# Performance work log

Measured on AMD Instinct MI355X. Metric: run time of the kernel, lower is better.

The kernel has to match this reference:

```python
import jax, jax.numpy as jnp
import numpy as np

HEAD, DIM, R = 8, 256, 3
RA = (2 * R + 1) ** 2  # 49


def conv2d(x, w, b=None, pad=0, groups=1):
    y = jax.lax.conv_general_dilated(x, w, (1, 1), [(pad, pad), (pad, pad)],
                                     dimension_numbers=('NCHW', 'OIHW', 'NCHW'),
                                     feature_group_count=groups)
    return y if b is None else y + b[None, :, None, None]


def grid_sample(img, grid, mode, padding='zeros'):
    # img [B,C,H,W]; grid [B,Hg,Wg,2] with (x,y) in [-1,1]; align_corners=False.
    B, C, H, W = img.shape
    Hg, Wg = grid.shape[1], grid.shape[2]
    gx = ((grid[..., 0] + 1.0) * W - 1.0) / 2.0
    gy = ((grid[..., 1] + 1.0) * H - 1.0) / 2.0
    if padding == 'border':
        gx = jnp.clip(gx, 0.0, W - 1.0)
        gy = jnp.clip(gy, 0.0, H - 1.0)
    gx = gx.reshape(B, -1)
    gy = gy.reshape(B, -1)

    def gather(iy, ix):
        iyc = jnp.clip(iy, 0, H - 1)
        ixc = jnp.clip(ix, 0, W - 1)
        return jax.vmap(lambda im, a, b: im[:, a, b])(img, iyc, ixc)  # [B,C,N]

    def mask(iy, ix):
        if padding == 'border':
            return jnp.ones(iy.shape, img.dtype)
        return ((ix >= 0) & (ix < W) & (iy >= 0) & (iy < H)).astype(img.dtype)

    if mode == 'nearest':
        ix = jnp.round(gx).astype(jnp.int32)
        iy = jnp.round(gy).astype(jnp.int32)
        out = gather(iy, ix) * mask(iy, ix)[:, None, :]
    else:  # bilinear
        x0f = jnp.floor(gx); y0f = jnp.floor(gy)
        wx = gx - x0f; wy = gy - y0f
        x0 = x0f.astype(jnp.int32); y0 = y0f.astype(jnp.int32)
        out = jnp.zeros((B, C, gx.shape[1]), img.dtype)
        for dx, dy, w in ((0, 0, (1 - wx) * (1 - wy)), (1, 0, wx * (1 - wy)),
                          (0, 1, (1 - wx) * wy), (1, 1, wx * wy)):
            ix = x0 + dx; iy = y0 + dy
            out = out + gather(iy, ix) * (w * mask(iy, ix))[:, None, :]
    return out.reshape(B, C, Hg, Wg)


def mlp2(x, W1, b1, W2, b2):
    return jax.nn.relu(x @ W1.T + b1) @ W2.T + b2


def setup_inputs() -> dict:
    key = jax.random.key(0)
    ks = jax.random.split(key, 32)
    B, H, W, Q = 1, 64, 64, 4096
    f32 = jnp.float32
    rn = lambda k, shp, s=0.02: jax.random.normal(k, shp, f32) * s
    return {
        'inp': jax.random.normal(ks[0], (B, 3, H, W), f32),
        'coord': jax.random.uniform(ks[1], (B, Q, 2), f32, -1.0, 1.0),
        'cell': jnp.full((B, Q, 2), 2.0 / (2 * H), f32),
        'W_enc': rn(ks[2], (64, 3, 3, 3)), 'b_enc': jnp.zeros((64,), f32),
        'W_ch': rn(ks[3], (256, 64, 3, 3)), 'b_ch': jnp.zeros((256,), f32),
        'W_q': rn(ks[4], (256, 256, 3, 3)), 'b_q': jnp.zeros((256,), f32),
        'W_k': rn(ks[5], (256, 256, 3, 3)), 'b_k': jnp.zeros((256,), f32),
        'W_v': rn(ks[6], (256, 256, 3, 3)), 'b_v': jnp.zeros((256,), f32),
        'W_off1': rn(ks[7], (256, 32, 5, 5)), 'b_off1': jnp.zeros((256,), f32),
        'ln_g': jnp.ones((256,), f32), 'ln_b': jnp.zeros((256,), f32),
        'W_off2': rn(ks[8], (98, 256, 1, 1)),
        'Wc1': rn(ks[9], (256, 98)), 'bc1': jnp.zeros((256,), f32),
        'Wc2': rn(ks[10], (49, 256)), 'bc2': jnp.zeros((49,), f32),
        'Wi1': rn(ks[11], (256, 12546)), 'bi1': jnp.zeros((256,), f32),
        'Wi2': rn(ks[12], (3, 256)), 'bi2': jnp.zeros((3,), f32),
        'scale': 2,
    }


def reference(inp, coord, cell, W_enc, b_enc, W_ch, b_ch, W_q, b_q, W_k, b_k,
              W_v, b_v, W_off1, b_off1, ln_g, ln_b, W_off2, Wc1, bc1, Wc2, bc2,
              Wi1, bi1, Wi2, bi2, scale):
    B, _, H, W = inp.shape
    Q = coord.shape[1]
    # gen_feat: encoder stub (conv+relu) -> conv_ch -> q/k/v convs
    feat = conv2d(jax.nn.relu(conv2d(inp, W_enc, b_enc, pad=1)), W_ch, b_ch, pad=1)
    fq = conv2d(feat, W_q, b_q, pad=1)
    fk = conv2d(feat, W_k, b_k, pad=1)
    fv = conv2d(feat, W_v, b_v, pad=1)
    # offset branch: grouped 5x5 conv -> channelwise LN -> GELU -> 1x1 conv (no bias)
    o = conv2d(feat, W_off1, b_off1, pad=2, groups=8)
    oc = o.transpose(0, 2, 3, 1)
    mu = oc.mean(-1, keepdims=True)
    var = ((oc - mu) ** 2).mean(-1, keepdims=True)
    oc = (oc - mu) / jnp.sqrt(var + 1e-5) * ln_g + ln_b
    offsets = conv2d(jax.nn.gelu(oc.transpose(0, 3, 1, 2), approximate=False), W_off2, None, pad=0)  # [B,98,H,W]
    # LR coordinate grid (y,x) at pixel centers in [-1,1]
    ys = -1.0 + 1.0 / H + (2.0 / H) * jnp.arange(H, dtype=inp.dtype)
    xs = -1.0 + 1.0 / W + (2.0 / W) * jnp.arange(W, dtype=inp.dtype)
    coord_lr = jnp.broadcast_to(jnp.stack(jnp.meshgrid(ys, xs, indexing='ij'), 0)[None], (B, 2, H, W))
    sc = coord[:, :, None, :]          # [B,Q,1,2] (y,x)
    g = sc[..., ::-1]                  # (x,y) for grid_sample
    sck = grid_sample(coord_lr, g, 'nearest').transpose(0, 2, 3, 1)  # [B,Q,1,2]
    off = grid_sample(offsets, g, 'nearest').transpose(0, 2, 3, 1).reshape(B, Q, RA, 2)
    off = jnp.tanh(off) * jnp.array([1.0 / (H - 1.0), 1.0 / (W - 1.0)], inp.dtype) * 2.0
    d = jnp.linspace(-R, R, 2 * R + 1).astype(inp.dtype)
    delta = jnp.stack(jnp.meshgrid(d * (2.0 / H), d * (2.0 / W), indexing='ij'), -1).reshape(1, 1, RA, 2)
    sck = sck + delta + off            # [B,Q,49,2] sampling locs (y,x)
    q = grid_sample(fq, g, 'bilinear').transpose(0, 2, 3, 1).reshape(B, Q, HEAD, DIM // HEAD)
    k = grid_sample(fk, sck[..., ::-1], 'nearest').transpose(0, 2, 3, 1).reshape(B, Q, RA, HEAD, DIM // HEAD)
    v = grid_sample(fv, sck[..., ::-1], 'nearest').transpose(0, 2, 3, 1).reshape(B, Q, RA, HEAD, DIM // HEAD)
    attn_val = jnp.einsum('bqhd,bqkhd->bqkh', q, k) / np.sqrt(DIM // HEAD)  # [B,Q,49,8]
    rel = (sc - sck) * jnp.array([H, W], inp.dtype)  # [B,Q,49,2]
    wcoord = mlp2(rel.reshape(B * Q, RA * 2), Wc1, bc1, Wc2, bc2).reshape(B, Q, RA, 1)
    attn = jax.nn.softmax(wcoord + attn_val, axis=2)  # softmax over 49 samples
    feat_in = (v * attn[..., None]).reshape(B, Q, RA * DIM)
    rel_cell = cell * jnp.array([H, W], inp.dtype)
    feat_in = jnp.concatenate([feat_in, rel_cell], -1)  # [B,Q,12546]
    pred = mlp2(feat_in.reshape(B * Q, -1), Wi1, bi1, Wi2, bi2).reshape(B, Q, 3)
    skip = grid_sample(inp, g, 'bilinear', 'border')[:, :, :, 0].transpose(0, 2, 1)
    return pred + skip
```

## Files before the change

kernel.cpp:

```cpp
#include <hip/hip_runtime.h>
#include <hip/hip_bf16.h>


typedef unsigned short u16;
typedef unsigned int u32;
using frag_ab = __attribute__((ext_vector_type(8))) short;
using frag_cd = __attribute__((ext_vector_type(4))) float;

#define HW 4096
#define NQ 4096
#define KBIG 12576
#define SPLITK 16
#define KCHUNK 800
#define JMAX 5
#define KQ 2304
#define QSPLIT 3
#define QCHUNK 768
#define NBLK_QKV (64 * 6 * QSPLIT)
#define NBLK_OFF1 (64 * 8)

static __device__ __forceinline__ u16 f2b(float f) {
  union { __hip_bfloat16 h; u16 u; } c; c.h = __float2bfloat16(f); return c.u;
}
static __device__ __forceinline__ float b2f(u16 v) {
  return __uint_as_float((u32)v << 16);
}
static __device__ __forceinline__ u32 pk2(float a, float b) {
  union { __hip_bfloat162 h; u32 u; } c;
  c.h = __float22bfloat162_rn(float2{a, b});
  return c.u;
}
static __device__ __forceinline__ void glds16(const u16* g, u16* l) {
  __builtin_amdgcn_global_load_lds(
      (const __attribute__((address_space(1))) u32*)(g),
      (__attribute__((address_space(3))) u32*)(l), 16, 0, 0);
}

#define BM 64
#define BN 64
#define BK 32
#define LDSS 40

__global__ __launch_bounds__(256)
void gemm_feat(const u16* __restrict__ feat, const u16* __restrict__ Btqkv,
               u16* __restrict__ Pq, const u16* __restrict__ Btoff1,
               float* __restrict__ obuf, const float* __restrict__ b_off1)
{
  __shared__ u16 smem[6656];
  const int bid = blockIdx.x;
  const int tid = threadIdx.x;
  const int wave = tid >> 6, lane = tid & 63;
  const int lr = lane & 15, lk = lane >> 4;

  if (bid < NBLK_QKV) {
    u16* As = smem;
    u16* Bs = smem + 64 * 40;
    const int mz  = bid & 63;
    const int rest = bid >> 6;
    const int ny  = rest % 6;
    const int z   = rest / 6;
    const int m0  = mz * 64;
    const int n0  = ny * 128;
    const int kbeg = z * QCHUNK;
    const int kend = kbeg + QCHUNK;
    const int nw = wave * 32;
    const int arow = tid >> 2, acol = (tid & 3) * 8;
    const int p = m0 + arow, y = p >> 6, x = p & 63;

    frag_cd acc[4][2] = {};
    const u16* bbase = Btqkv + (size_t)(n0 + (tid >> 2)) * KQ + (tid & 3) * 8 + kbeg;
    u16* bdst = &Bs[(size_t)tid * 8];

    auto stageA = [&](int k0) -> uint4 {
      int k = k0 + acol;
      int s = k >> 8, c = k & 255;
      int dy = s / 3, dx = s - dy * 3;
      int yy = y + dy - 1, xx = x + dx - 1;
      if (((unsigned)yy < 64u) && ((unsigned)xx < 64u))
        return *(const uint4*)&feat[(size_t)(yy * 64 + xx) * 256 + c];
      return uint4{0u, 0u, 0u, 0u};
    };

    uint4 av = stageA(kbeg);

    for (int k0 = kbeg; k0 < kend; k0 += BK) {
      glds16(bbase + (k0 - kbeg), bdst);
      glds16(bbase + (k0 - kbeg) + (size_t)64 * KQ, bdst + 2048);
      *(uint4*)&As[arow * LDSS + acol] = av;
      __syncthreads();
      if (k0 + BK < kend) av = stageA(k0 + BK);
      frag_ab af[4];
      #pragma unroll
      for (int i = 0; i < 4; i++)
        af[i] = *(const frag_ab*)&As[(i * 16 + lr) * LDSS + lk * 8];
      #pragma unroll
      for (int j = 0; j < 2; j++) {
        frag_ab bf = *(const frag_ab*)&Bs[(nw + j * 16 + lr) * 32 + lk * 8];
        #pragma unroll
        for (int i = 0; i < 4; i++)
          acc[i][j] = __builtin_amdgcn_mfma_f32_16x16x32_bf16(af[i], bf, acc[i][j], 0, 0, 0);
      }
      __syncthreads();
    }

    #pragma unroll
    for (int i = 0; i < 4; i++)
      #pragma unroll
      for (int j = 0; j < 2; j++) {
        int col = n0 + nw + j * 16 + lr;
        #pragma unroll
        for (int r = 0; r < 4; r++) {
          int row = m0 + i * 16 + lk * 4 + r;
          Pq[(size_t)z * (NQ * 768) + (size_t)row * 768 + col] = f2b(acc[i][j][r]);
        }
      }
  } else {
    u16* As = smem;
    u16* Bs = smem + 64 * 40;
    const int t  = bid - NBLK_QKV;
    const int m0 = (t & 63) * 64;
    const int g  = t >> 6;
    const int cb = g * 32;
    const u16* Bt = Btoff1 + (size_t)g * 32 * 800;
    const float* bz = b_off1 + g * 32;
    const int mw = (wave & 1) * 32, nw = (wave >> 1) * 32;
    const int srow = tid >> 2, scol = (tid & 3) * 8;
    const int p = m0 + srow, y = p >> 6, x = p & 63;

    frag_cd acc[2][2] = {};
    const bool bok  = srow < 32;
    const u16* bptr = Bt + (size_t)srow * 800 + scol;

    auto stageA = [&](int k0) -> uint4 {
      int k = k0 + scol;
      int s = k >> 5;
      int c = k & 31;
      int dy = s / 5, dx = s - dy * 5;
      int yy = y + dy - 2, xx = x + dx - 2;
      if (((unsigned)yy < 64u) && ((unsigned)xx < 64u))
        return *(const uint4*)&feat[(size_t)(yy * 64 + xx) * 256 + cb + c];
      return uint4{0u, 0u, 0u, 0u};
    };

    uint4 av = stageA(0);
    uint4 bv = bok ? *(const uint4*)(bptr) : uint4{0u, 0u, 0u, 0u};

    for (int k0 = 0; k0 < 800; k0 += BK) {
      *(uint4*)&As[srow * LDSS + scol] = av;
      *(uint4*)&Bs[srow * LDSS + scol] = bv;
      __syncthreads();
      if (k0 + BK < 800) {
        av = stageA(k0 + BK);
        bv = bok ? *(const uint4*)(bptr + k0 + BK) : uint4{0u, 0u, 0u, 0u};
      }
      frag_ab af0 = *(const frag_ab*)&As[(mw      + lr) * LDSS + lk * 8];
      frag_ab af1 = *(const frag_ab*)&As[(mw + 16 + lr) * LDSS + lk * 8];
      frag_ab bf0 = *(const frag_ab*)&Bs[(nw      + lr) * LDSS + lk * 8];
      frag_ab bf1 = *(const frag_ab*)&Bs[(nw + 16 + lr) * LDSS + lk * 8];
      acc[0][0] = __builtin_amdgcn_mfma_f32_16x16x32_bf16(af0, bf0, acc[0][0], 0, 0, 0);
      acc[0][1] = __builtin_amdgcn_mfma_f32_16x16x32_bf16(af0, bf1, acc[0][1], 0, 0, 0);
      acc[1][0] = __builtin_amdgcn_mfma_f32_16x16x32_bf16(af1, bf0, acc[1][0], 0, 0, 0);
      acc[1][1] = __builtin_amdgcn_mfma_f32_16x16x32_bf16(af1, bf1, acc[1][1], 0, 0, 0);
      __syncthreads();
    }

    #pragma unroll
    for (int i = 0; i < 2; i++)
      #pragma unroll
      for (int j = 0; j < 2; j++) {
        int col = nw + j * 16 + lr;
        if (col >= 32) continue;
        float badd = bz[col];
        #pragma unroll
        for (int r = 0; r < 4; r++) {
          int row = m0 + mw + i * 16 + lk * 4 + r;
          obuf[(size_t)row * 256 + g * 32 + col] = acc[i][j][r] + badd;
        }
      }
  }
}

#define RQ_BLKS 1536
#define LNO_BLKS 256
__global__ __launch_bounds__(256)
void post_feat(const u16* __restrict__ P, const float* __restrict__ bias,
               u16* __restrict__ outQ, u16* __restrict__ outK,
               u16* __restrict__ outV,
               const float* __restrict__ x, const float* __restrict__ g,
               const float* __restrict__ b, const u16* __restrict__ Btoff2,
               float* __restrict__ offsb)
{
  __shared__ u16 s_oc[16 * 264];
  const int bid = blockIdx.x;
  const int tid = threadIdx.x;
  if (bid < RQ_BLKS) {
    int i8 = bid * 256 + tid;
    size_t i = (size_t)i8 * 8;
    int row = (int)(i / 768);
    int c = (int)(i % 768);
    float v[8];
    #pragma unroll
    for (int t = 0; t < 8; t++) v[t] = bias[c + t];
    for (int z = 0; z < QSPLIT; z++) {
      uint4 a = *(const uint4*)&P[(size_t)z * (NQ * 768) + i];
      u32 aw[4] = {a.x, a.y, a.z, a.w};
      #pragma unroll
      for (int t = 0; t < 4; t++) {
        v[2 * t]     += __uint_as_float(aw[t] << 16);
        v[2 * t + 1] += __uint_as_float(aw[t] & 0xffff0000u);
      }
    }
    uint4 ob = {pk2(v[0], v[1]), pk2(v[2], v[3]), pk2(v[4], v[5]), pk2(v[6], v[7])};
    if (c < 256) {
      *(uint4*)&outQ[(size_t)row * 256 + c] = ob;
    } else if (c < 512) {
      *(uint4*)&outK[(size_t)row * 256 + (c - 256)] = ob;
    } else {
      *(uint4*)&outV[(size_t)row * 256 + (c - 512)] = ob;
    }
  } else {
    const int p0 = (bid - RQ_BLKS) * 16;
    const int p = tid >> 4, gl = tid & 15;
    float v[16];
    {
      const float* src = x + (size_t)(p0 + p) * 256 + gl * 16;
      #pragma unroll
      for (int t = 0; t < 4; t++) {
        float4 f = *(const float4*)(src + t * 4);
        v[4 * t] = f.x; v[4 * t + 1] = f.y; v[4 * t + 2] = f.z; v[4 * t + 3] = f.w;
      }
    }
    float s1 = 0.f, s2 = 0.f;
    #pragma unroll
    for (int t = 0; t < 16; t++) { s1 += v[t]; s2 += v[t] * v[t]; }
    #pragma unroll
    for (int off = 8; off; off >>= 1) {
      s1 += __shfl_xor(s1, off, 16);
      s2 += __shfl_xor(s2, off, 16);
    }
    float mu   = s1 * (1.f / 256.f);
    float var  = s2 * (1.f / 256.f) - mu * mu;
    float rstd = rsqrtf(var + 1e-5f);
    #pragma unroll
    for (int t = 0; t < 16; t++) {
      int c = gl * 16 + t;
      float xn = (v[t] - mu) * rstd * g[c] + b[c];
      float ge = 0.5f * xn * (1.f + erff(xn * 0.70710678118654752f));
      s_oc[p * 264 + c] = f2b(ge);
    }
    __syncthreads();
    const int wave = tid >> 6, lane = tid & 63;
    const int lr = lane & 15, lk = lane >> 4;
    frag_cd a0 = {}, a1 = {};
    #pragma unroll
    for (int k0 = 0; k0 < 256; k0 += 32) {
      frag_ab af = *(const frag_ab*)&s_oc[lr * 264 + k0 + lk * 8];
      frag_ab bf0 = *(const frag_ab*)&Btoff2[(size_t)(wave * 16 + lr) * 256 + k0 + lk * 8];
      a0 = __builtin_amdgcn_mfma_f32_16x16x32_bf16(af, bf0, a0, 0, 0, 0);
      if (wave < 3) {
        frag_ab bf1 = *(const frag_ab*)&Btoff2[(size_t)((wave + 4) * 16 + lr) * 256 + k0 + lk * 8];
        a1 = __builtin_amdgcn_mfma_f32_16x16x32_bf16(af, bf1, a1, 0, 0, 0);
      }
    }
    {
      const int col0 = wave * 16 + lr;
      const int col1 = (wave + 4) * 16 + lr;
      #pragma unroll
      for (int r = 0; r < 4; r++) {
        int row = lk * 4 + r;
        offsb[(size_t)(p0 + row) * 98 + col0] = a0[r];
        if (wave < 3 && col1 < 98)
          offsb[(size_t)(p0 + row) * 98 + col1] = a1[r];
      }
    }
  }
}

__global__ __launch_bounds__(512, 4)
void gemm_big(const u16* __restrict__ Bt, const u16* __restrict__ fqkvV,
              const float* __restrict__ attnval, const int* __restrict__ vidx,
              const float* __restrict__ cell, u16* __restrict__ P)
{
  __shared__ u16 As[128 * LDSS];
  __shared__ u16 Bs[2 * 256 * 32];
  __shared__ short s_vidx[JMAX * 128];
  __shared__ float s_attn[JMAX * 128 * 8];
  const int tid  = threadIdx.x;
  const int m0   = blockIdx.x * 128;
  const int z    = blockIdx.y;
  const int kbeg = z * KCHUNK;
  const int kend = min(KBIG, kbeg + KCHUNK);
  const int jbeg = kbeg >> 8;
  const int jcnt = ((kend - 1) >> 8) - jbeg + 1;
  const int wave = tid >> 6, lane = tid & 63;
  const int mw = (wave & 1) * 64, nwv = (wave >> 1) * 64;
  const int lr = lane & 15, lk = lane >> 4;
  const int arow = tid >> 2, acol = (tid & 3) * 8;
  const int q = m0 + arow;

  for (int t = tid; t < 128 * jcnt; t += 512) {
    int r = t & 127, jj = t >> 7;
    int j = jbeg + jj;
    s_vidx[t] = (short)((j < 49) ? vidx[(m0 + r) * 49 + j] : -1);
  }
  for (int t = tid; t < 128 * 8 * jcnt; t += 512) {
    int h = t & 7, rr = (t >> 3) & 127, jj = t >> 10;
    int j = jbeg + jj;
    s_attn[t] = (j < 49) ? attnval[((size_t)((m0 + rr) * 49 + j)) * 8 + h] : 0.f;
  }
  __syncthreads();

  auto loadA = [&](int k0, uint4& kv, float& w) {
    const int k = k0 + acol;
    const int j = k >> 8, c = k & 255;
    kv = uint4{0u, 0u, 0u, 0u};
    w = 0.f;
    if (j < 49) {
      const int jj = j - jbeg;
      int id = s_vidx[jj * 128 + arow];
      if (id >= 0) {
        w = s_attn[(jj * 128 + arow) * 8 + (c >> 5)];
        kv = *(const uint4*)(fqkvV + (size_t)id * 256 + c);
      }
    } else if (c == 0) {
      kv.x = pk2(cell[q * 2], cell[q * 2 + 1]);
      w = 64.f;
    }
  };

  frag_cd acc[4][4] = {};
  uint4 kvc; float wc_;
  const u16* bbase = Bt + (size_t)(tid >> 2) * KBIG + (tid & 3) * 8 + kbeg;

  glds16(bbase, &Bs[(size_t)tid * 8]);
  glds16(bbase + (size_t)128 * KBIG, &Bs[(size_t)tid * 8 + 4096]);
  loadA(kbeg, kvc, wc_);

  int par = 0;
  for (int k0 = kbeg; k0 < kend; k0 += BK, par ^= 1) {
    {
      u32 aw[4] = {kvc.x, kvc.y, kvc.z, kvc.w};
      uint4 av;
      u32 avw[4];
      #pragma unroll
      for (int t = 0; t < 4; t++) {
        float lo = __uint_as_float(aw[t] << 16) * wc_;
        float hi = __uint_as_float(aw[t] & 0xffff0000u) * wc_;
        avw[t] = pk2(lo, hi);
      }
      av.x = avw[0]; av.y = avw[1]; av.z = avw[2]; av.w = avw[3];
      *(uint4*)&As[arow * LDSS + acol] = av;
    }
    if (k0 + BK < kend) {
      u16* bd = &Bs[(size_t)(par ^ 1) * 8192 + (size_t)tid * 8];
      glds16(bbase + (k0 + BK - kbeg), bd);
      glds16(bbase + (k0 + BK - kbeg) + (size_t)128 * KBIG, bd + 4096);
      asm volatile("s_waitcnt vmcnt(2) lgkmcnt(0)" ::: "memory");
    } else {
      asm volatile("s_waitcnt vmcnt(0) lgkmcnt(0)" ::: "memory");
    }
    __builtin_amdgcn_s_barrier();
    if (k0 + BK < kend) loadA(k0 + BK, kvc, wc_);
    const u16* bsrc = &Bs[(size_t)par * 8192];
    frag_ab af[4];
    #pragma unroll
    for (int i = 0; i < 4; i++)
      af[i] = *(const frag_ab*)&As[(mw + i * 16 + lr) * LDSS + lk * 8];
    #pragma unroll
    for (int j = 0; j < 4; j++) {
      frag_ab bf = *(const frag_ab*)&bsrc[(nwv + j * 16 + lr) * 32 + lk * 8];
      #pragma unroll
      for (int i = 0; i < 4; i++)
        acc[i][j] = __builtin_amdgcn_mfma_f32_16x16x32_bf16(af[i], bf, acc[i][j], 0, 0, 0);
    }
    asm volatile("s_waitcnt lgkmcnt(0)" ::: "memory");
    __builtin_amdgcn_s_barrier();
  }

  #pragma unroll
  for (int i = 0; i < 4; i++)
    #pragma unroll
    for (int j = 0; j < 4; j++) {
      int col = nwv + j * 16 + lr;
      #pragma unroll
      for (int r = 0; r < 4; r++) {
        int row = m0 + mw + i * 16 + lk * 4 + r;
        P[(size_t)z * (NQ * 256) + (size_t)row * 256 + col] = f2b(acc[i][j][r]);
      }
    }
}

__global__ __launch_bounds__(256)
void reduce_final(const u16* __restrict__ Pb, const float* __restrict__ bi1,
                  const float* __restrict__ Wi2, const float* __restrict__ bi2,
                  const float* __restrict__ skipb, float* __restrict__ out)
{
  const int q = blockIdx.x, c = threadIdx.x;
  float s = 0.f;
  #pragma unroll
  for (int z = 0; z < SPLITK; z++)
    s += b2f(Pb[(size_t)z * (NQ * 256) + (size_t)q * 256 + c]);
  s += bi1[c];
  s = fmaxf(s, 0.f);

  __shared__ float part[3][4];
  float p0 = s * Wi2[c], p1 = s * Wi2[256 + c], p2 = s * Wi2[512 + c];
  #pragma unroll
  for (int off = 32; off; off >>= 1) {
    p0 += __shfl_xor(p0, off);
    p1 += __shfl_xor(p1, off);
    p2 += __shfl_xor(p2, off);
  }
  if ((c & 63) == 0) {
    int w = c >> 6;
    part[0][w] = p0; part[1][w] = p1; part[2][w] = p2;
  }
  __syncthreads();
  if (c < 3)
    out[q * 3 + c] = bi2[c] + skipb[q * 3 + c]
                   + part[c][0] + part[c][1] + part[c][2] + part[c][3];
}

__global__ __launch_bounds__(256)
void attn_wc(const u16* __restrict__ relbuf, const u16* __restrict__ Btc1,
             const float* __restrict__ bc1, const u16* __restrict__ Btc2,
             const float* __restrict__ bc2, float* __restrict__ attnval)
{
  __shared__ u16 s_rel[16 * 136];
  __shared__ u16 s_hid[16 * 264];
  __shared__ float s_wc[16 * 52];
  const int tid = threadIdx.x;
  const int m0 = blockIdx.x * 16;
  const int wave = tid >> 6, lane = tid & 63;
  const int lr = lane & 15, lk = lane >> 4;

  {
    int r = tid >> 4, kc = (tid & 15) * 8;
    uint4 v = *(const uint4*)&relbuf[(size_t)(m0 + r) * 128 + kc];
    *(uint4*)&s_rel[r * 136 + kc] = v;
  }
  __syncthreads();

  frag_cd acc1[4] = {};
  #pragma unroll
  for (int k0 = 0; k0 < 128; k0 += 32) {
    frag_ab af = *(const frag_ab*)&s_rel[lr * 136 + k0 + lk * 8];
    #pragma unroll
    for (int j = 0; j < 4; j++) {
      int col = wave * 64 + j * 16 + lr;
      frag_ab bf = *(const frag_ab*)&Btc1[(size_t)col * 128 + k0 + lk * 8];
      acc1[j] = __builtin_amdgcn_mfma_f32_16x16x32_bf16(af, bf, acc1[j], 0, 0, 0);
    }
  }
  #pragma unroll
  for (int j = 0; j < 4; j++) {
    int col = wave * 64 + j * 16 + lr;
    float badd = bc1[col];
    #pragma unroll
    for (int r = 0; r < 4; r++) {
      int row = lk * 4 + r;
      s_hid[row * 264 + col] = f2b(fmaxf(acc1[j][r] + badd, 0.f));
    }
  }
  __syncthreads();

  frag_cd acc2 = {};
  #pragma unroll
  for (int k0 = 0; k0 < 256; k0 += 32) {
    frag_ab af = *(const frag_ab*)&s_hid[lr * 264 + k0 + lk * 8];
    frag_ab bf = *(const frag_ab*)&Btc2[(size_t)(wave * 16 + lr) * 256 + k0 + lk * 8];
    acc2 = __builtin_amdgcn_mfma_f32_16x16x32_bf16(af, bf, acc2, 0, 0, 0);
  }
  {
    int col = wave * 16 + lr;
    if (col < 49) {
      float badd = bc2[col];
      #pragma unroll
      for (int r = 0; r < 4; r++) {
        int row = lk * 4 + r;
        s_wc[row * 52 + col] = acc2[r] + badd;
      }
    }
  }
  __syncthreads();

  if (tid < 128) {
    const int qq = tid >> 3, h = tid & 7;
    float* avp = attnval + ((size_t)(m0 + qq) * 49) * 8 + h;
    float v[49];
    float m = -1e30f;
    #pragma unroll
    for (int l = 0; l < 49; l++) {
      v[l] = s_wc[qq * 52 + l] + avp[(size_t)l * 8];
      m = fmaxf(m, v[l]);
    }
    float ssum = 0.f;
    #pragma unroll
    for (int l = 0; l < 49; l++) { v[l] = expf(v[l] - m); ssum += v[l]; }
    float inv = 1.f / ssum;
    #pragma unroll
    for (int l = 0; l < 49; l++) avp[(size_t)l * 8] = v[l] * inv;
  }
}

static __device__ __forceinline__
void packconv(const float* __restrict__ W, u16* __restrict__ Bt,
              int Cin, int K2, int idx)
{
  int o  = idx / (Cin * K2);
  int r  = idx - o * (Cin * K2);
  int ci = r / K2;
  int s  = r - ci * K2;
  Bt[(size_t)o * (Cin * K2) + s * Cin + ci] = f2b(W[idx]);
}
static __device__ __forceinline__
void packcast(const float* __restrict__ W, u16* __restrict__ Bt,
              int Kin, int Kout, int idx)
{
  int n = idx / Kout, k = idx - n * Kout;
  Bt[idx] = f2b(k < Kin ? W[(size_t)n * Kin + k] : 0.f);
}

#define SZ_CH    147456
#define SZ_QKV   589824
#define SZ_OFF1  204800
#define SZ_OFF2P 28672
#define SZ_C1    32768
#define SZ_C2P   16384
#define SZ_WI1   3219456
#define SZ_REST (3*SZ_QKV + SZ_OFF1 + SZ_OFF2P + SZ_C1 + SZ_C2P + 768 + SZ_WI1)
#define CONV_BLKS 1024
#define CONV2_BLKS 256

__global__ __launch_bounds__(256)
void pack_enc(const float* __restrict__ inp, const float* __restrict__ W_enc,
              const float* __restrict__ b_enc, u16* __restrict__ feat1,
              const float* __restrict__ W_ch, u16* __restrict__ Btch)
{
  const int bid = blockIdx.x;
  const int tid = threadIdx.x;
  if (bid < CONV_BLKS) {
    const int p = bid * 4 + (tid >> 6), c = tid & 63;
    const int y = p >> 6, x = p & 63;
    float s = b_enc[c];
    #pragma unroll
    for (int ci = 0; ci < 3; ci++)
      #pragma unroll
      for (int dy = 0; dy < 3; dy++) {
        int yy = y + dy - 1;
        if ((unsigned)yy >= 64u) continue;
        #pragma unroll
        for (int dx = 0; dx < 3; dx++) {
          int xx = x + dx - 1;
          if ((unsigned)xx >= 64u) continue;
          s += inp[ci * HW + yy * 64 + xx] * W_enc[((c * 3 + ci) * 3 + dy) * 3 + dx];
        }
      }
    feat1[(size_t)p * 64 + c] = f2b(fmaxf(s, 0.f));
    return;
  }
  int i = (bid - CONV_BLKS) * 256 + tid;
  if (i < SZ_CH) packconv(W_ch, Btch, 64, 9, i);
}

__global__ __launch_bounds__(256)
void conv_pack(const u16* __restrict__ feat1, const u16* __restrict__ Btch,
               u16* __restrict__ feat, const float* __restrict__ b_ch,
               const float* W_q, const float* W_k, const float* W_v,
               const float* W_off1, const float* W_off2,
               const float* Wc1, const float* Wc2, const float* Wi1,
               const float* b_q, const float* b_k, const float* b_v,
               u16* Btqkv, u16* Btoff1, u16* Btoff2,
               u16* Btc1, u16* Btc2, u16* Wi1p, float* bqkv)
{
  __shared__ u16 As[BM * LDSS];
  __shared__ u16 Bs[BN * LDSS];
  const int bid = blockIdx.x;
  const int tid = threadIdx.x;
  if (bid < CONV2_BLKS) {
    const int m0 = (bid & 63) * 64;
    const int n0 = (bid >> 6) * 64;
    const int wave = tid >> 6, lane = tid & 63;
    const int mw = (wave & 1) * 32, nw = (wave >> 1) * 32;
    const int lr = lane & 15, lk = lane >> 4;
    const int srow = tid >> 2, scol = (tid & 3) * 8;
    const int p = m0 + srow, y = p >> 6, x = p & 63;

    frag_cd acc[2][2] = {};
    const u16* bptr = Btch + (size_t)(n0 + srow) * 576 + scol;

    auto stageA = [&](int k0) -> uint4 {
      int k = k0 + scol;
      int s = k >> 6;
      int c = k & 63;
      int dy = s / 3, dx = s - dy * 3;
      int yy = y + dy - 1, xx = x + dx - 1;
      if (((unsigned)yy < 64u) && ((unsigned)xx < 64u))
        return *(const uint4*)&feat1[(size_t)(yy * 64 + xx) * 64 + c];
      return uint4{0u, 0u, 0u, 0u};
    };

    uint4 av = stageA(0);
    uint4 bv = *(const uint4*)(bptr);

    for (int k0 = 0; k0 < 576; k0 += BK) {
      *(uint4*)&As[srow * LDSS + scol] = av;
      *(uint4*)&Bs[srow * LDSS + scol] = bv;
      __syncthreads();
      if (k0 + BK < 576) {
        av = stageA(k0 + BK);
        bv = *(const uint4*)(bptr + k0 + BK);
      }
      frag_ab af0 = *(const frag_ab*)&As[(mw      + lr) * LDSS + lk * 8];
      frag_ab af1 = *(const frag_ab*)&As[(mw + 16 + lr) * LDSS + lk * 8];
      frag_ab bf0 = *(const frag_ab*)&Bs[(nw      + lr) * LDSS + lk * 8];
      frag_ab bf1 = *(const frag_ab*)&Bs[(nw + 16 + lr) * LDSS + lk * 8];
      acc[0][0] = __builtin_amdgcn_mfma_f32_16x16x32_bf16(af0, bf0, acc[0][0], 0, 0, 0);
      acc[0][1] = __builtin_amdgcn_mfma_f32_16x16x32_bf16(af0, bf1, acc[0][1], 0, 0, 0);
      acc[1][0] = __builtin_amdgcn_mfma_f32_16x16x32_bf16(af1, bf0, acc[1][0], 0, 0, 0);
      acc[1][1] = __builtin_amdgcn_mfma_f32_16x16x32_bf16(af1, bf1, acc[1][1], 0, 0, 0);
      __syncthreads();
    }

    #pragma unroll
    for (int i = 0; i < 2; i++)
      #pragma unroll
      for (int j = 0; j < 2; j++) {
        int col = n0 + nw + j * 16 + lr;
        float badd = b_ch[col];
        #pragma unroll
        for (int r = 0; r < 4; r++) {
          int row = m0 + mw + i * 16 + lk * 4 + r;
          feat[(size_t)row * 256 + col] = f2b(acc[i][j][r] + badd);
        }
      }
    return;
  }
  int i = (bid - CONV2_BLKS) * 256 + tid;
  if (i < SZ_QKV) { packconv(W_q, Btqkv, 256, 9, i); return; }
  i -= SZ_QKV;
  if (i < SZ_QKV) { packconv(W_k, Btqkv + (size_t)256 * 2304, 256, 9, i); return; }
  i -= SZ_QKV;
  if (i < SZ_QKV) { packconv(W_v, Btqkv + (size_t)512 * 2304, 256, 9, i); return; }
  i -= SZ_QKV;
  if (i < SZ_OFF1) { packconv(W_off1, Btoff1, 32, 25, i); return; }
  i -= SZ_OFF1;
  if (i < SZ_OFF2P) {
    int n = i >> 8, k = i & 255;
    Btoff2[i] = f2b(n < 98 ? W_off2[n * 256 + k] : 0.f);
    return;
  }
  i -= SZ_OFF2P;
  if (i < SZ_C1) { packcast(Wc1, Btc1, 98, 128, i); return; }
  i -= SZ_C1;
  if (i < SZ_C2P) {
    int n = i >> 8, k = i & 255;
    Btc2[i] = f2b(n < 49 ? Wc2[n * 256 + k] : 0.f);
    return;
  }
  i -= SZ_C2P;
  if (i < 768) {
    bqkv[i] = (i < 256) ? b_q[i] : (i < 512) ? b_k[i - 256] : b_v[i - 512];
    return;
  }
  i -= 768;
  if (i < SZ_WI1) { packcast(Wi1, Wi1p, 12546, 12576, i); }
}

__global__ __launch_bounds__(256)
void sampler(const float* __restrict__ coord, const u16* __restrict__ fqkvQb,
             const u16* __restrict__ fqkvKb,
             const float* __restrict__ offs, const float* __restrict__ inp,
             float* __restrict__ attnval, u16* __restrict__ relbuf,
             int* __restrict__ vidx, float* __restrict__ skipb)
{
  const int q = blockIdx.x;
  const int tid = threadIdx.x;
  __shared__ float s_off[98];
  __shared__ int s_idx[49];
  __shared__ float s_q[256];

  const float c0 = coord[q * 2], c1 = coord[q * 2 + 1];
  const float gxp = ((c1 + 1.f) * 64.f - 1.f) * 0.5f;
  const float gyp = ((c0 + 1.f) * 64.f - 1.f) * 0.5f;
  const int ixn = (int)rintf(gxp), iyn = (int)rintf(gyp);
  const bool inn = ((unsigned)ixn < 64u) && ((unsigned)iyn < 64u);

  if (tid < 98) {
    float v = inn ? offs[(size_t)(iyn * 64 + ixn) * 98 + tid] : 0.f;
    s_off[tid] = tanhf(v) * (2.f / 63.f);
  }
  __syncthreads();

  const float scky = inn ? (-1.f + (float)(2 * iyn + 1) * (1.f / 64.f)) : 0.f;
  const float sckx = inn ? (-1.f + (float)(2 * ixn + 1) * (1.f / 64.f)) : 0.f;

  if (tid < 49) {
    const int a = tid / 7, bb = tid - a * 7;
    float sy = scky + (float)(a - 3) * (2.f / 64.f) + s_off[2 * tid];
    float sx = sckx + (float)(bb - 3) * (2.f / 64.f) + s_off[2 * tid + 1];
    relbuf[(size_t)q * 128 + 2 * tid]     = f2b((c0 - sy) * 64.f);
    relbuf[(size_t)q * 128 + 2 * tid + 1] = f2b((c1 - sx) * 64.f);
    float gx2 = ((sx + 1.f) * 64.f - 1.f) * 0.5f;
    float gy2 = ((sy + 1.f) * 64.f - 1.f) * 0.5f;
    int ix2 = (int)rintf(gx2), iy2 = (int)rintf(gy2);
    int id = (((unsigned)ix2 < 64u) && ((unsigned)iy2 < 64u)) ? (iy2 * 64 + ix2) : -1;
    s_idx[tid] = id;
    vidx[q * 49 + tid] = id;
  } else if (tid >= 98 && tid < 128) {
    relbuf[(size_t)q * 128 + tid] = 0;
  }

  {
    const float x0f = floorf(gxp), y0f = floorf(gyp);
    const float wx = gxp - x0f, wy = gyp - y0f;
    const int x0 = (int)x0f, y0 = (int)y0f;
    float qc = 0.f;
    #pragma unroll
    for (int t = 0; t < 4; t++) {
      int xi = x0 + (t & 1), yi = y0 + (t >> 1);
      if (((unsigned)xi < 64u) && ((unsigned)yi < 64u)) {
        float w = ((t & 1) ? wx : 1.f - wx) * ((t >> 1) ? wy : 1.f - wy);
        qc += w * b2f(fqkvQb[(size_t)(yi * 64 + xi) * 256 + tid]);
      }
    }
    s_q[tid] = qc * 0.17677669529663687f;
  }

  if (tid < 3) {
    float gx = fminf(fmaxf(gxp, 0.f), 63.f);
    float gy = fminf(fmaxf(gyp, 0.f), 63.f);
    float xf = floorf(gx), yf = floorf(gy);
    float wxs = gx - xf, wys = gy - yf;
    int xa = (int)xf, ya = (int)yf;
    int xb = min(xa + 1, 63), yb = min(ya + 1, 63);
    const float* ch = inp + tid * HW;
    float v = (1.f - wxs) * (1.f - wys) * ch[ya * 64 + xa]
            + wxs * (1.f - wys) * ch[ya * 64 + xb]
            + (1.f - wxs) * wys * ch[yb * 64 + xa]
            + wxs * wys * ch[yb * 64 + xb];
    skipb[q * 3 + tid] = v;
  }
  __syncthreads();

  const int wave = tid >> 6, lane = tid & 63;
  const int half = lane >> 5, sub = lane & 31;
  const int ch0 = sub * 8;
  const int h = sub >> 2;
  float qv[8];
  #pragma unroll
  for (int i = 0; i < 8; i++) qv[i] = s_q[ch0 + i];

  for (int it = 0; it < 7; it++) {
    int j = it * 8 + wave * 2 + half;
    if (j >= 49) break;
    int id = s_idx[j];
    float p = 0.f;
    if (id >= 0) {
      uint4 kv = *(const uint4*)&fqkvKb[(size_t)id * 256 + ch0];
      u32 w0 = kv.x, w1 = kv.y, w2 = kv.z, w3 = kv.w;
      p = fmaf(qv[0], __uint_as_float(w0 << 16), p);
      p = fmaf(qv[1], __uint_as_float(w0 & 0xffff0000u), p);
      p = fmaf(qv[2], __uint_as_float(w1 << 16), p);
      p = fmaf(qv[3], __uint_as_float(w1 & 0xffff0000u), p);
      p = fmaf(qv[4], __uint_as_float(w2 << 16), p);
      p = fmaf(qv[5], __uint_as_float(w2 & 0xffff0000u), p);
      p = fmaf(qv[6], __uint_as_float(w3 << 16), p);
      p = fmaf(qv[7], __uint_as_float(w3 & 0xffff0000u), p);
    }
    p += __shfl_down(p, 2, 4);
    p += __shfl_down(p, 1, 4);
    if ((sub & 3) == 0) attnval[((size_t)q * 49 + j) * 8 + h] = p;
  }
}

extern "C" void kernel_launch(void* const* d_in, const int* in_sizes, int n_in,
                              void* d_out, int out_size, void* d_ws, size_t ws_size,
                              hipStream_t stream)
{
  const float* inp    = (const float*)d_in[0];
  const float* coord  = (const float*)d_in[1];
  const float* cell   = (const float*)d_in[2];
  const float* W_enc  = (const float*)d_in[3];
  const float* b_enc  = (const float*)d_in[4];
  const float* W_ch   = (const float*)d_in[5];
  const float* b_ch   = (const float*)d_in[6];
  const float* W_q    = (const float*)d_in[7];
  const float* b_q    = (const float*)d_in[8];
  const float* W_k    = (const float*)d_in[9];
  const float* b_k    = (const float*)d_in[10];
  const float* W_v    = (const float*)d_in[11];
  const float* b_v    = (const float*)d_in[12];
  const float* W_off1 = (const float*)d_in[13];
  const float* b_off1 = (const float*)d_in[14];
  const float* ln_g   = (const float*)d_in[15];
  const float* ln_b   = (const float*)d_in[16];
  const float* W_off2 = (const float*)d_in[17];
  const float* Wc1    = (const float*)d_in[18];
  const float* bc1    = (const float*)d_in[19];
  const float* Wc2    = (const float*)d_in[20];
  const float* bc2    = (const float*)d_in[21];
  const float* Wi1    = (const float*)d_in[22];
  const float* bi1    = (const float*)d_in[23];
  const float* Wi2    = (const float*)d_in[24];
  const float* bi2    = (const float*)d_in[25];

  char* base = (char*)d_ws;
  size_t off = 0;
  auto alloc = [&](size_t bytes) -> char* {
    char* r = base + off;
    off = (off + bytes + 255) & ~(size_t)255;
    return r;
  };

  float* obuf   = (float*)alloc((size_t)HW * 256 * 4);
  float* offsb  = (float*)alloc((size_t)HW * 98 * 4);
  u16*   feat1  = (u16*)  alloc((size_t)HW * 64 * 2);
  u16*   feat   = (u16*)  alloc((size_t)HW * 256 * 2);
  u16*   relbuf = (u16*)  alloc((size_t)NQ * 128 * 2);
  u16*   Btqkv  = (u16*)  alloc((size_t)768 * 2304 * 2);
  u16*   Btch   = (u16*)  alloc((size_t)256 * 576 * 2);
  u16*   Btoff1 = (u16*)  alloc((size_t)256 * 800 * 2);
  u16*   Btoff2 = (u16*)  alloc((size_t)112 * 256 * 2);
  u16*   Btc1   = (u16*)  alloc((size_t)256 * 128 * 2);
  u16*   Btc2   = (u16*)  alloc((size_t)64 * 256 * 2);
  u16* Pb = (u16*)base;
  u16* Pqb = (u16*)(base + ((size_t)36 << 20));
  {
    size_t need = ((size_t)36 << 20) + (size_t)QSPLIT * NQ * 768 * 2;
    if (off < need) off = (need + 255) & ~(size_t)255;
  }
  u16*   fqkvQb  = (u16*)  alloc((size_t)HW * 256 * 2);
  u16*   fqkvKb  = (u16*)  alloc((size_t)HW * 256 * 2);
  u16*   fqkvVb  = (u16*)  alloc((size_t)HW * 256 * 2);
  float* attnval = (float*)alloc((size_t)NQ * 49 * 8 * 4);
  int*   vidxb   = (int*)  alloc((size_t)NQ * 49 * 4);
  float* skipb   = (float*)alloc((size_t)NQ * 3 * 4);
  u16*   Wi1p    = (u16*)  alloc((size_t)256 * KBIG * 2);
  float* bqkv    = (float*)alloc(768 * 4);
  (void)ws_size; (void)in_sizes; (void)n_in; (void)out_size;

  pack_enc<<<CONV_BLKS + (SZ_CH + 255) / 256, 256, 0, stream>>>(
      inp, W_enc, b_enc, feat1, W_ch, Btch);

  conv_pack<<<CONV2_BLKS + (SZ_REST + 255) / 256, 256, 0, stream>>>(
      feat1, Btch, feat, b_ch,
      W_q, W_k, W_v, W_off1, W_off2, Wc1, Wc2, Wi1, b_q, b_k, b_v,
      Btqkv, Btoff1, Btoff2, Btc1, Btc2, Wi1p, bqkv);

  gemm_feat<<<NBLK_QKV + NBLK_OFF1, 256, 0, stream>>>(
      feat, Btqkv, Pqb, Btoff1, obuf, b_off1);
  post_feat<<<RQ_BLKS + LNO_BLKS, 256, 0, stream>>>(
      Pqb, bqkv, fqkvQb, fqkvKb, fqkvVb, obuf, ln_g, ln_b, Btoff2, offsb);

  sampler<<<NQ, 256, 0, stream>>>(coord, fqkvQb, fqkvKb, offsb, inp,
                                  attnval, relbuf, vidxb, skipb);
  attn_wc<<<NQ / 16, 256, 0, stream>>>(relbuf, Btc1, bc1, Btc2, bc2, attnval);

  gemm_big<<<dim3(32, SPLITK), 512, 0, stream>>>(
      Wi1p, fqkvVb, attnval, vidxb, cell, Pb);
  reduce_final<<<NQ, 256, 0, stream>>>(Pb, bi1, Wi2, bi2, skipb, (float*)d_out);
}
```

Before: 258.1 us.

## Split gemm_big N dimension into two 128-wide tiles with 256-thread blocks

The big split-K GEMM now launches a 3D grid with two N tiles of 128 columns per block, using 256 threads instead of 512, and halves the B shared-memory buffer. Each thread stages 16 A elements instead of 8, and attention weights are read straight from global memory instead of being preloaded into shared memory. This doubles the block count and cuts LDS use per block to raise occupancy, but each N tile recomputes the gathered and weighted A tile, doubling those global gathers.

```diff
diff --git a/kernel.cpp b/kernel.cpp
--- a/kernel.cpp
+++ b/kernel.cpp
@@ -276,18 +276,18 @@
   }
 }
 
-__global__ __launch_bounds__(512, 4)
+__global__ __launch_bounds__(256, 4)
 void gemm_big(const u16* __restrict__ Bt, const u16* __restrict__ fqkvV,
               const float* __restrict__ attnval, const int* __restrict__ vidx,
               const float* __restrict__ cell, u16* __restrict__ P)
 {
   __shared__ u16 As[128 * LDSS];
-  __shared__ u16 Bs[2 * 256 * 32];
+  __shared__ u16 Bs[2 * 128 * 32];
   __shared__ short s_vidx[JMAX * 128];
-  __shared__ float s_attn[JMAX * 128 * 8];
   const int tid  = threadIdx.x;
   const int m0   = blockIdx.x * 128;
-  const int z    = blockIdx.y;
+  const int n0   = blockIdx.y * 128;
+  const int z    = blockIdx.z;
   const int kbeg = z * KCHUNK;
   const int kend = min(KBIG, kbeg + KCHUNK);
   const int jbeg = kbeg >> 8;
@@ -295,73 +295,77 @@
   const int wave = tid >> 6, lane = tid & 63;
   const int mw = (wave & 1) * 64, nwv = (wave >> 1) * 64;
   const int lr = lane & 15, lk = lane >> 4;
-  const int arow = tid >> 2, acol = (tid & 3) * 8;
+  const int arow = tid >> 1, acol = (tid & 1) * 16;
   const int q = m0 + arow;
 
-  for (int t = tid; t < 128 * jcnt; t += 512) {
+  for (int t = tid; t < 128 * jcnt; t += 256) {
     int r = t & 127, jj = t >> 7;
     int j = jbeg + jj;
     s_vidx[t] = (short)((j < 49) ? vidx[(m0 + r) * 49 + j] : -1);
   }
-  for (int t = tid; t < 128 * 8 * jcnt; t += 512) {
-    int h = t & 7, rr = (t >> 3) & 127, jj = t >> 10;
-    int j = jbeg + jj;
-    s_attn[t] = (j < 49) ? attnval[((size_t)((m0 + rr) * 49 + j)) * 8 + h] : 0.f;
-  }
   __syncthreads();
 
-  auto loadA = [&](int k0, uint4& kv, float& w) {
+  auto loadA = [&](int k0, uint4& kv0, uint4& kv1, float& w) {
     const int k = k0 + acol;
     const int j = k >> 8, c = k & 255;
-    kv = uint4{0u, 0u, 0u, 0u};
+    kv0 = uint4{0u, 0u, 0u, 0u};
+    kv1 = uint4{0u, 0u, 0u, 0u};
     w = 0.f;
     if (j < 49) {
       const int jj = j - jbeg;
       int id = s_vidx[jj * 128 + arow];
       if (id >= 0) {
-        w = s_attn[(jj * 128 + arow) * 8 + (c >> 5)];
-        kv = *(const uint4*)(fqkvV + (size_t)id * 256 + c);
+        w = attnval[((size_t)(q * 49 + j)) * 8 + (c >> 5)];
+        const u16* src = fqkvV + (size_t)id * 256 + c;
+        kv0 = *(const uint4*)(src);
+        kv1 = *(const uint4*)(src + 8);
       }
     } else if (c == 0) {
-      kv.x = pk2(cell[q * 2], cell[q * 2 + 1]);
+      kv0.x = pk2(cell[q * 2], cell[q * 2 + 1]);
       w = 64.f;
     }
   };
 
+  auto stage = [&](const uint4& kv0, const uint4& kv1, float w) {
+    u32 aw0[4] = {kv0.x, kv0.y, kv0.z, kv0.w};
+    u32 aw1[4] = {kv1.x, kv1.y, kv1.z, kv1.w};
+    uint4 av0, av1;
+    u32 w0[4], w1[4];
+    #pragma unroll
+    for (int t = 0; t < 4; t++) {
+      w0[t] = pk2(__uint_as_float(aw0[t] << 16) * w,
+                  __uint_as_float(aw0[t] & 0xffff0000u) * w);
+      w1[t] = pk2(__uint_as_float(aw1[t] << 16) * w,
+                  __uint_as_float(aw1[t] & 0xffff0000u) * w);
+    }
+    av0.x = w0[0]; av0.y = w0[1]; av0.z = w0[2]; av0.w = w0[3];
+    av1.x = w1[0]; av1.y = w1[1]; av1.z = w1[2]; av1.w = w1[3];
+    *(uint4*)&As[arow * LDSS + acol]     = av0;
+    *(uint4*)&As[arow * LDSS + acol + 8] = av1;
+  };
+
   frag_cd acc[4][4] = {};
-  uint4 kvc; float wc_;
-  const u16* bbase = Bt + (size_t)(tid >> 2) * KBIG + (tid & 3) * 8 + kbeg;
+  uint4 kc0, kc1; float wc_;
+  const u16* bbase = Bt + (size_t)(n0 + (tid >> 2)) * KBIG + (tid & 3) * 8 + kbeg;
 
   glds16(bbase, &Bs[(size_t)tid * 8]);
-  glds16(bbase + (size_t)128 * KBIG, &Bs[(size_t)tid * 8 + 4096]);
-  loadA(kbeg, kvc, wc_);
+  glds16(bbase + (size_t)64 * KBIG, &Bs[(size_t)tid * 8 + 2048]);
+  loadA(kbeg, kc0, kc1, wc_);
 
   int par = 0;
   for (int k0 = kbeg; k0 < kend; k0 += BK, par ^= 1) {
-    {
-      u32 aw[4] = {kvc.x, kvc.y, kvc.z, kvc.w};
-      uint4 av;
-      u32 avw[4];
-      #pragma unroll
-      for (int t = 0; t < 4; t++) {
-        float lo = __uint_as_float(aw[t] << 16) * wc_;
-        float hi = __uint_as_float(aw[t] & 0xffff0000u) * wc_;
-        avw[t] = pk2(lo, hi);
-      }
-      av.x = avw[0]; av.y = avw[1]; av.z = avw[2]; av.w = avw[3];
-      *(uint4*)&As[arow * LDSS + acol] = av;
-    }
+    stage(kc0, kc1, wc_);
     if (k0 + BK < kend) {
-      u16* bd = &Bs[(size_t)(par ^ 1) * 8192 + (size_t)tid * 8];
+      u16* bd = &Bs[(size_t)(par ^ 1) * 4096 + (size_t)tid * 8];
       glds16(bbase + (k0 + BK - kbeg), bd);
-      glds16(bbase + (k0 + BK - kbeg) + (size_t)128 * KBIG, bd + 4096);
+      glds16(bbase + (k0 + BK - kbeg) + (size_t)64 * KBIG, bd + 2048);
       asm volatile("s_waitcnt vmcnt(2) lgkmcnt(0)" ::: "memory");
     } else {
       asm volatile("s_waitcnt vmcnt(0) lgkmcnt(0)" ::: "memory");
     }
     __builtin_amdgcn_s_barrier();
-    if (k0 + BK < kend) loadA(k0 + BK, kvc, wc_);
-    const u16* bsrc = &Bs[(size_t)par * 8192];
+    if (k0 + BK < kend) loadA(k0 + BK, kc0, kc1, wc_);
+    const u16* bsrc = &Bs[(size_t)par * 4096];
     frag_ab af[4];
     #pragma unroll
     for (int i = 0; i < 4; i++)
@@ -381,7 +385,7 @@
   for (int i = 0; i < 4; i++)
     #pragma unroll
     for (int j = 0; j < 4; j++) {
-      int col = nwv + j * 16 + lr;
+      int col = n0 + nwv + j * 16 + lr;
       #pragma unroll
       for (int r = 0; r < 4; r++) {
         int row = m0 + mw + i * 16 + lk * 4 + r;
@@ -857,7 +861,7 @@
                                   attnval, relbuf, vidxb, skipb);
   attn_wc<<<NQ / 16, 256, 0, stream>>>(relbuf, Btc1, bc1, Btc2, bc2, attnval);
 
-  gemm_big<<<dim3(32, SPLITK), 512, 0, stream>>>(
+  gemm_big<<<dim3(32, 2, SPLITK), 256, 0, stream>>>(
       Wi1p, fqkvVb, attnval, vidxb, cell, Pb);
   reduce_final<<<NQ, 256, 0, stream>>>(Pb, bi1, Wi2, bi2, skipb, (float*)d_out);
 }
```

After: 268.3 us. +4.0%, slower.
